# Kernel optimization log

Measured on AMD Instinct MI355X. Metric: run time of the kernel, lower is better.

The kernel has to match this reference:

```python
import jax, jax.numpy as jnp
import numpy as np

FEATURE_DIM = 128
EDGE_DIM = 32
N_NODES = 10000
BATCH = 4
N_EDGES = 640000
TEMPERATURE = 0.66
POWER_ITERS = 5


def spectral_normalize(W):
    # torch.nn.utils.spectral_norm: divide W by largest singular value estimated
    # via power iteration; u, v are treated as constants (no grad).
    # W: [out, in]
    u = jnp.ones((W.shape[0],), W.dtype) / jnp.sqrt(jnp.asarray(W.shape[0], W.dtype))
    for _ in range(POWER_ITERS):
        v = W.T @ u
        v = v / (jnp.linalg.norm(v) + 1e-12)
        u = W @ v
        u = u / (jnp.linalg.norm(u) + 1e-12)
    u = jax.lax.stop_gradient(u)
    v = jax.lax.stop_gradient(v)
    sigma = u @ (W @ v)
    return W / sigma


def setup_inputs() -> dict:
    key = jax.random.key(0)
    ks = jax.random.split(key, 8)
    node_feat = jax.random.normal(ks[0], (BATCH, N_NODES, FEATURE_DIM), dtype=jnp.float32)
    batch_ids = jax.random.randint(ks[1], (N_EDGES,), 0, BATCH)
    src_nodes = jax.random.randint(ks[2], (N_EDGES,), 0, N_NODES)
    tgt_nodes = jax.random.randint(ks[3], (N_EDGES,), 0, N_NODES)
    in_dim = 2 * FEATURE_DIM + 1  # src_feat ++ tgt_feat ++ distance
    # kaiming_normal_(nonlinearity='relu'): std = sqrt(2 / fan_in)
    W1 = jax.random.normal(ks[4], (EDGE_DIM, in_dim), jnp.float32) * np.sqrt(2.0 / in_dim)
    b1 = jnp.zeros((EDGE_DIM,), jnp.float32)
    W2 = jax.random.normal(ks[5], (EDGE_DIM, EDGE_DIM), jnp.float32) * np.sqrt(2.0 / EDGE_DIM)
    b2 = jnp.zeros((EDGE_DIM,), jnp.float32)
    bound = 0.1 * np.sqrt(6.0 / (EDGE_DIM + 1))
    W3 = jax.random.uniform(ks[6], (1, EDGE_DIM), jnp.float32, -bound, bound)
    b3 = jnp.ones((1,), jnp.float32)
    return {"node_feat": node_feat, "W1": W1, "b1": b1, "W2": W2, "b2": b2,
            "W3": W3, "b3": b3, "batch_ids": batch_ids,
            "src_nodes": src_nodes, "tgt_nodes": tgt_nodes}


def reference(node_feat, W1, b1, W2, b2, W3, b3, batch_ids, src_nodes, tgt_nodes):
    # per-edge gather of endpoint features  [E, D]
    src_feat = node_feat[batch_ids, src_nodes]
    tgt_feat = node_feat[batch_ids, tgt_nodes]
    dist = jnp.linalg.norm(src_feat - tgt_feat, axis=-1, keepdims=True)  # [E,1]
    edge_features = jnp.concatenate([src_feat, tgt_feat, dist], axis=-1)  # [E, 2D+1]
    # spectral-norm MLP (dropout is identity at eval / in this reference)
    h = jax.nn.relu(edge_features @ spectral_normalize(W1).T + b1)
    h = jax.nn.relu(h @ spectral_normalize(W2).T + b2)
    logAlpha = (h @ spectral_normalize(W3).T + b3).squeeze(-1)  # [E]
    logAlpha = jnp.clip(logAlpha, -5.0, 5.0)
    edge_weights = jax.nn.sigmoid(logAlpha / TEMPERATURE)
    return edge_weights, logAlpha
```

## Files before the change

### kernel.cpp

```cpp
#include <hip/hip_runtime.h>
#include <hip/hip_fp16.h>
#include <math.h>

#define FEATD 128
#define NNODES 10000
#define NBATCH 4
#define NROWS (NBATCH*NNODES)

#define OFF_I1   0
#define OFF_W1L  8
#define OFF_W2   64
#define OFF_W3   1088
#define OFF_W2H  1120
#define OFF_P16  4096
#define P16_FLOATS (NROWS*64/2)
#define OFF_FQ   (OFF_P16 + P16_FLOATS)
#define F16_FLOATS (NROWS*FEATD/2)
#define OFF_FBWT OFF_P16

#define WSTRIDE 68

typedef _Float16 h2 __attribute__((ext_vector_type(2)));
union U32H2 { unsigned u; h2 h; };
union U4H2  { uint4 u; h2 h[4]; };

#if defined(__has_builtin)
#if __has_builtin(__builtin_amdgcn_fdot2)
#define HAVE_FDOT2 1
#endif
#if __has_builtin(__builtin_amdgcn_cvt_pk_f32_fp8) && __has_builtin(__builtin_amdgcn_cvt_pk_fp8_f32)
#define HAVE_FP8 1
#endif
#endif

__device__ __forceinline__ float fdot2f(h2 a, h2 b, float c) {
#ifdef HAVE_FDOT2
  return __builtin_amdgcn_fdot2(a, b, c, false);
#else
  return c + (float)a[0] * (float)b[0] + (float)a[1] * (float)b[1];
#endif
}

#ifdef HAVE_FP8
typedef float floatx2 __attribute__((ext_vector_type(2)));
__device__ __forceinline__ float ssd_fp8_w(unsigned aw, unsigned bw, float s) {
  floatx2 al = __builtin_amdgcn_cvt_pk_f32_fp8((int)aw, false);
  floatx2 ah = __builtin_amdgcn_cvt_pk_f32_fp8((int)aw, true);
  floatx2 bl = __builtin_amdgcn_cvt_pk_f32_fp8((int)bw, false);
  floatx2 bh = __builtin_amdgcn_cvt_pk_f32_fp8((int)bw, true);
  float d0 = al[0] - bl[0], d1 = al[1] - bl[1];
  float d2 = ah[0] - bh[0], d3 = ah[1] - bh[1];
  return s + d0 * d0 + d1 * d1 + d2 * d2 + d3 * d3;
}
__device__ __forceinline__ float grp_dist_fp8(uint2 au, uint2 bu) {
  float ssd = ssd_fp8_w(au.x, bu.x, 0.f);
  ssd = ssd_fp8_w(au.y, bu.y, ssd);
  ssd += __shfl_xor(ssd, 1, 64);
  ssd += __shfl_xor(ssd, 2, 64);
  ssd += __shfl_xor(ssd, 4, 64);
  ssd += __shfl_xor(ssd, 8, 64);
  return sqrtf(ssd);
}
#endif

template <int M, int K>
__device__ float spectral_sigma_t(const float* __restrict__ Wg,
                                  float* sW, float* u, float* v, volatile float* red) {
  int tid = threadIdx.x;
  int wid = tid >> 6, lid = tid & 63;
  int j8 = tid >> 3, l8 = tid & 7;
  for (int i = tid; i < M * K; i += 256) sW[i] = Wg[i];
  if (tid < M) u[tid] = 1.0f;
  __syncthreads();
  float invu = 1.0f / sqrtf((float)M);
  float invv = 0.f;

  for (int it = 0; it < 5; ++it) {
    float p = 0.f;
    for (int k = tid; k < K; k += 256) {
      float a = 0.f;
      #pragma unroll
      for (int j = 0; j < M; ++j) a += sW[j * K + k] * u[j];
      a *= invu;
      v[k] = a;
      p += a * a;
    }
    #pragma unroll
    for (int off = 1; off < 64; off <<= 1) p += __shfl_xor(p, off, 64);
    if (lid == 0) red[wid] = p;
    __syncthreads();
    p = red[0] + red[1] + red[2] + red[3];
    invv = 1.0f / (sqrtf(p) + 1e-12f);

    float a = 0.f;
    if (j8 < M) {
      #pragma unroll
      for (int k = l8; k < K; k += 8) a += sW[j8 * K + k] * v[k];
      a *= invv;
    }
    a += __shfl_xor(a, 1, 64);
    a += __shfl_xor(a, 2, 64);
    a += __shfl_xor(a, 4, 64);
    float q = 0.f;
    if (j8 < M && l8 == 0) { u[j8] = a; q = a * a; }
    #pragma unroll
    for (int off = 1; off < 64; off <<= 1) q += __shfl_xor(q, off, 64);
    if (lid == 0) red[4 + wid] = q;
    __syncthreads();
    q = red[4] + red[5] + red[6] + red[7];
    invu = 1.0f / (sqrtf(q) + 1e-12f);
  }

  float a = 0.f;
  if (j8 < M) {
    #pragma unroll
    for (int k = l8; k < K; k += 8) a += sW[j8 * K + k] * v[k];
  }
  a += __shfl_xor(a, 1, 64);
  a += __shfl_xor(a, 2, 64);
  a += __shfl_xor(a, 4, 64);
  float s = (j8 < M && l8 == 0) ? a * u[j8] : 0.f;
  #pragma unroll
  for (int off = 1; off < 64; off <<= 1) s += __shfl_xor(s, off, 64);
  if (lid == 0) red[wid] = s;
  __syncthreads();
  float sig = (red[0] + red[1] + red[2] + red[3]) * invu * invv;
  __syncthreads();
  return sig;
}

__global__ __launch_bounds__(256, 4) void prep_kernel(const float* __restrict__ feat,
                                                      const float* __restrict__ W1,
                                                      const float* __restrict__ W2,
                                                      const float* __restrict__ W3,
                                                      float* __restrict__ ws,
                                                      int doFQ) {
  __shared__ float sA[128 * WSTRIDE];
  __shared__ float u[32], v[257];
  __shared__ float red[8];
  int tid = threadIdx.x;

  if (blockIdx.x == 0) {
    float sig1 = spectral_sigma_t<32, 257>(W1, sA, u, v, red);
    float i1 = 1.0f / sig1;
    if (tid == 0) ws[OFF_I1] = i1;
    for (int j = tid; j < 32; j += 256) ws[OFF_W1L + j] = sA[j * 257 + 256] * i1;
    __syncthreads();
    float sig2 = spectral_sigma_t<32, 32>(W2, sA, u, v, red);
    float i2 = 1.0f / sig2;
    for (int idx = tid; idx < 1024; idx += 256) ws[OFF_W2 + idx] = sA[idx] * i2;
    unsigned* w2h = (unsigned*)(ws + OFF_W2H);
    for (int idx = tid; idx < 512; idx += 256) {
      int j = idx >> 4, q = idx & 15;
      U32H2 pk;
      pk.h[0] = (_Float16)(sA[j * 32 + 2 * q] * i2);
      pk.h[1] = (_Float16)(sA[j * 32 + 2 * q + 1] * i2);
      w2h[idx] = pk.u;
    }
    __syncthreads();
    float sig3 = spectral_sigma_t<1, 32>(W3, sA, u, v, red);
    float i3 = 1.0f / sig3;
    for (int k = tid; k < 32; k += 256) ws[OFF_W3 + k] = sA[k] * i3;
    return;
  }

  for (int idx = tid; idx < 32 * 257; idx += 256) {
    int j = idx / 257, c = idx - j * 257;
    float w = W1[idx];
    if (c < 128) sA[c * WSTRIDE + j] = w;
    else if (c < 256) sA[(c - 128) * WSTRIDE + 32 + j] = w;
  }
  __syncthreads();

  __half* p16 = (__half*)(ws + OFF_P16);
  char* fq = (char*)(ws + OFF_FQ);
  int rg = tid >> 4;
  int jg = (tid & 15) << 2;
  int slice = tid & 15;
  int r0 = (blockIdx.x - 1) * 64 + rg * 4;
  const float4* F0 = (const float4*)&feat[(size_t)(r0 + 0) * FEATD];
  const float4* F1 = (const float4*)&feat[(size_t)(r0 + 1) * FEATD];
  const float4* F2 = (const float4*)&feat[(size_t)(r0 + 2) * FEATD];
  const float4* F3 = (const float4*)&feat[(size_t)(r0 + 3) * FEATD];
  float acc[4][4] = {{0,0,0,0},{0,0,0,0},{0,0,0,0},{0,0,0,0}};

  #pragma unroll 2
  for (int k4 = 0; k4 < 32; ++k4) {
    float4 f0 = F0[k4], f1 = F1[k4], f2 = F2[k4], f3 = F3[k4];
    if (doFQ && (k4 >> 1) == slice) {
#ifdef HAVE_FP8
      unsigned w;
      w = __builtin_amdgcn_cvt_pk_fp8_f32(f0.x, f0.y, 0, false);
      w = __builtin_amdgcn_cvt_pk_fp8_f32(f0.z, f0.w, (int)w, true);
      *(unsigned*)(fq + (size_t)(r0 + 0) * 128 + (size_t)k4 * 4) = w;
      w = __builtin_amdgcn_cvt_pk_fp8_f32(f1.x, f1.y, 0, false);
      w = __builtin_amdgcn_cvt_pk_fp8_f32(f1.z, f1.w, (int)w, true);
      *(unsigned*)(fq + (size_t)(r0 + 1) * 128 + (size_t)k4 * 4) = w;
      w = __builtin_amdgcn_cvt_pk_fp8_f32(f2.x, f2.y, 0, false);
      w = __builtin_amdgcn_cvt_pk_fp8_f32(f2.z, f2.w, (int)w, true);
      *(unsigned*)(fq + (size_t)(r0 + 2) * 128 + (size_t)k4 * 4) = w;
      w = __builtin_amdgcn_cvt_pk_fp8_f32(f3.x, f3.y, 0, false);
      w = __builtin_amdgcn_cvt_pk_fp8_f32(f3.z, f3.w, (int)w, true);
      *(unsigned*)(fq + (size_t)(r0 + 3) * 128 + (size_t)k4 * 4) = w;
#else
      U32H2 a, b; uint2 pk;
      a.h[0]=(_Float16)f0.x; a.h[1]=(_Float16)f0.y; b.h[0]=(_Float16)f0.z; b.h[1]=(_Float16)f0.w;
      pk.x=a.u; pk.y=b.u; *(uint2*)(fq + (size_t)(r0+0)*256 + (size_t)k4*8) = pk;
      a.h[0]=(_Float16)f1.x; a.h[1]=(_Float16)f1.y; b.h[0]=(_Float16)f1.z; b.h[1]=(_Float16)f1.w;
      pk.x=a.u; pk.y=b.u; *(uint2*)(fq + (size_t)(r0+1)*256 + (size_t)k4*8) = pk;
      a.h[0]=(_Float16)f2.x; a.h[1]=(_Float16)f2.y; b.h[0]=(_Float16)f2.z; b.h[1]=(_Float16)f2.w;
      pk.x=a.u; pk.y=b.u; *(uint2*)(fq + (size_t)(r0+2)*256 + (size_t)k4*8) = pk;
      a.h[0]=(_Float16)f3.x; a.h[1]=(_Float16)f3.y; b.h[0]=(_Float16)f3.z; b.h[1]=(_Float16)f3.w;
      pk.x=a.u; pk.y=b.u; *(uint2*)(fq + (size_t)(r0+3)*256 + (size_t)k4*8) = pk;
#endif
    }
    #pragma unroll
    for (int kk = 0; kk < 4; ++kk) {
      int k = 4 * k4 + kk;
      float4 w = *(const float4*)&sA[k * WSTRIDE + jg];
      float e0 = (kk == 0) ? f0.x : (kk == 1) ? f0.y : (kk == 2) ? f0.z : f0.w;
      float e1 = (kk == 0) ? f1.x : (kk == 1) ? f1.y : (kk == 2) ? f1.z : f1.w;
      float e2 = (kk == 0) ? f2.x : (kk == 1) ? f2.y : (kk == 2) ? f2.z : f2.w;
      float e3 = (kk == 0) ? f3.x : (kk == 1) ? f3.y : (kk == 2) ? f3.z : f3.w;
      acc[0][0] += e0 * w.x; acc[0][1] += e0 * w.y; acc[0][2] += e0 * w.z; acc[0][3] += e0 * w.w;
      acc[1][0] += e1 * w.x; acc[1][1] += e1 * w.y; acc[1][2] += e1 * w.z; acc[1][3] += e1 * w.w;
      acc[2][0] += e2 * w.x; acc[2][1] += e2 * w.y; acc[2][2] += e2 * w.z; acc[2][3] += e2 * w.w;
      acc[3][0] += e3 * w.x; acc[3][1] += e3 * w.y; acc[3][2] += e3 * w.z; acc[3][3] += e3 * w.w;
    }
  }
  #pragma unroll
  for (int r = 0; r < 4; ++r) {
    U32H2 a, b;
    a.h[0] = (_Float16)acc[r][0]; a.h[1] = (_Float16)acc[r][1];
    b.h[0] = (_Float16)acc[r][2]; b.h[1] = (_Float16)acc[r][3];
    uint2 o; o.x = a.u; o.y = b.u;
    *(uint2*)((char*)p16 + (size_t)(r0 + r) * 128 + (size_t)jg * 2) = o;
  }
}

__device__ __forceinline__ float grp_dist_f16(uint4 au, uint4 bu) {
  U4H2 a, b; a.u = au; b.u = bu;
  float ssd = 0.f;
  #pragma unroll
  for (int p = 0; p < 4; ++p) { h2 d = a.h[p] - b.h[p]; ssd = fdot2f(d, d, ssd); }
  ssd += __shfl_xor(ssd, 1, 64);
  ssd += __shfl_xor(ssd, 2, 64);
  ssd += __shfl_xor(ssd, 4, 64);
  ssd += __shfl_xor(ssd, 8, 64);
  return sqrtf(ssd);
}

__device__ __forceinline__ unsigned h1pack(unsigned puv, unsigned quv, float dist, float i1,
                                           float w1l0, float w1l1, float bb0, float bb1) {
  U32H2 p, q; p.u = puv; q.u = quv;
  float h0  = fmaxf(fmaf((float)p.h[0] + (float)q.h[0], i1, fmaf(dist, w1l0, bb0)), 0.f);
  float h1v = fmaxf(fmaf((float)p.h[1] + (float)q.h[1], i1, fmaf(dist, w1l1, bb1)), 0.f);
  U32H2 r; r.h[0] = (_Float16)h0; r.h[1] = (_Float16)h1v;
  return r.u;
}

template <bool FQ>
__global__ __launch_bounds__(256, 8) void edge_wave(const float* __restrict__ feat,
                                                    const float* __restrict__ ws,
                                                    const float* __restrict__ b1,
                                                    const float* __restrict__ b2,
                                                    const float* __restrict__ b3,
                                                    const int* __restrict__ bids,
                                                    const int* __restrict__ srcs,
                                                    const int* __restrict__ tgts,
                                                    float* __restrict__ out, int E) {
  __shared__ unsigned ht[4 * 64 * 17];
  int tid = threadIdx.x;
  int wv   = tid >> 6;
  int l64  = tid & 63;
  int grp  = l64 >> 4;
  int lane = l64 & 15;
  unsigned* htw = &ht[wv * 64 * 17];

  const char*  featq = (const char*)(ws + OFF_FQ);
  const __half* p16  = (const __half*)(ws + OFF_P16);
  const unsigned* w2h = (const unsigned*)(ws + OFF_W2H);

  float i1 = ws[OFF_I1];
  int j0 = 2 * lane;
  float w1l0 = ws[OFF_W1L + j0];
  float w1l1 = ws[OFF_W1L + j0 + 1];
  float bb0  = b1[j0];
  float bb1  = b1[j0 + 1];
  float bias3 = b3[0];

  int wstep = gridDim.x * 4 * 64;
  for (int base = (blockIdx.x * 4 + wv) * 64; base < E; base += wstep) {
    int e = base + l64;
    int rs_m = 0, rt_m = 0;
    if (e < E) {
      int b = bids[e];
      rs_m = b * NNODES + srcs[e];
      rt_m = b * NNODES + tgts[e];
    }

    if (FQ && (base + 64 <= E)) {
      int elb = grp << 4;
      #pragma unroll 1
      for (int rr = 0; rr < 4; ++rr) {
        int el0 = elb + 4 * rr + 0;
        int el1 = elb + 4 * rr + 1;
        int el2 = elb + 4 * rr + 2;
        int el3 = elb + 4 * rr + 3;
        int rs0 = __shfl(rs_m, el0, 64), rt0 = __shfl(rt_m, el0, 64);
        int rs1 = __shfl(rs_m, el1, 64), rt1 = __shfl(rt_m, el1, 64);
        int rs2 = __shfl(rs_m, el2, 64), rt2 = __shfl(rt_m, el2, 64);
        int rs3 = __shfl(rs_m, el3, 64), rt3 = __shfl(rt_m, el3, 64);
#ifdef HAVE_FP8
        uint2 a0 = *(const uint2*)(featq + ((size_t)rs0 << 7) + (lane << 3));
        uint2 c0 = *(const uint2*)(featq + ((size_t)rt0 << 7) + (lane << 3));
        uint2 a1 = *(const uint2*)(featq + ((size_t)rs1 << 7) + (lane << 3));
        uint2 c1 = *(const uint2*)(featq + ((size_t)rt1 << 7) + (lane << 3));
        uint2 a2 = *(const uint2*)(featq + ((size_t)rs2 << 7) + (lane << 3));
        uint2 c2 = *(const uint2*)(featq + ((size_t)rt2 << 7) + (lane << 3));
        uint2 a3 = *(const uint2*)(featq + ((size_t)rs3 << 7) + (lane << 3));
        uint2 c3 = *(const uint2*)(featq + ((size_t)rt3 << 7) + (lane << 3));
#else
        uint4 a0 = *(const uint4*)(featq + ((size_t)rs0 << 8) + (lane << 4));
        uint4 c0 = *(const uint4*)(featq + ((size_t)rt0 << 8) + (lane << 4));
        uint4 a1 = *(const uint4*)(featq + ((size_t)rs1 << 8) + (lane << 4));
        uint4 c1 = *(const uint4*)(featq + ((size_t)rt1 << 8) + (lane << 4));
        uint4 a2 = *(const uint4*)(featq + ((size_t)rs2 << 8) + (lane << 4));
        uint4 c2 = *(const uint4*)(featq + ((size_t)rt2 << 8) + (lane << 4));
        uint4 a3 = *(const uint4*)(featq + ((size_t)rs3 << 8) + (lane << 4));
        uint4 c3 = *(const uint4*)(featq + ((size_t)rt3 << 8) + (lane << 4));
#endif
        unsigned pu0 = *(const unsigned*)((const char*)p16 + ((size_t)rs0 << 7) + (lane << 2));
        unsigned qu0 = *(const unsigned*)((const char*)p16 + ((size_t)rt0 << 7) + 64 + (lane << 2));
        unsigned pu1 = *(const unsigned*)((const char*)p16 + ((size_t)rs1 << 7) + (lane << 2));
        unsigned qu1 = *(const unsigned*)((const char*)p16 + ((size_t)rt1 << 7) + 64 + (lane << 2));
        unsigned pu2 = *(const unsigned*)((const char*)p16 + ((size_t)rs2 << 7) + (lane << 2));
        unsigned qu2 = *(const unsigned*)((const char*)p16 + ((size_t)rt2 << 7) + 64 + (lane << 2));
        unsigned pu3 = *(const unsigned*)((const char*)p16 + ((size_t)rs3 << 7) + (lane << 2));
        unsigned qu3 = *(const unsigned*)((const char*)p16 + ((size_t)rt3 << 7) + 64 + (lane << 2));
#ifdef HAVE_FP8
        float d0 = grp_dist_fp8(a0, c0);
        float d1 = grp_dist_fp8(a1, c1);
        float d2 = grp_dist_fp8(a2, c2);
        float d3 = grp_dist_fp8(a3, c3);
#else
        float d0 = grp_dist_f16(a0, c0);
        float d1 = grp_dist_f16(a1, c1);
        float d2 = grp_dist_f16(a2, c2);
        float d3 = grp_dist_f16(a3, c3);
#endif
        htw[el0 * 17 + lane] = h1pack(pu0, qu0, d0, i1, w1l0, w1l1, bb0, bb1);
        htw[el1 * 17 + lane] = h1pack(pu1, qu1, d1, i1, w1l0, w1l1, bb0, bb1);
        htw[el2 * 17 + lane] = h1pack(pu2, qu2, d2, i1, w1l0, w1l1, bb0, bb1);
        htw[el3 * 17 + lane] = h1pack(pu3, qu3, d3, i1, w1l0, w1l1, bb0, bb1);
      }
    } else {
      int elb = grp << 4;
      #pragma unroll 2
      for (int r = 0; r < 16; ++r) {
        int el = elb + r;
        if (base + el < E) {
          int rs = __shfl(rs_m, el, 64), rt = __shfl(rt_m, el, 64);
          float dist;
          if (FQ) {
#ifdef HAVE_FP8
            uint2 au = *(const uint2*)(featq + ((size_t)rs << 7) + (lane << 3));
            uint2 bu = *(const uint2*)(featq + ((size_t)rt << 7) + (lane << 3));
            dist = grp_dist_fp8(au, bu);
#else
            uint4 au = *(const uint4*)(featq + ((size_t)rs << 8) + (lane << 4));
            uint4 bu = *(const uint4*)(featq + ((size_t)rt << 8) + (lane << 4));
            dist = grp_dist_f16(au, bu);
#endif
          } else {
            const float4* A  = (const float4*)&feat[(size_t)rs * FEATD];
            const float4* Bp = (const float4*)&feat[(size_t)rt * FEATD];
            float ssd = 0.f;
            #pragma unroll
            for (int p = 0; p < 2; ++p) {
              float4 a = A[lane * 2 + p], c = Bp[lane * 2 + p];
              float dx = a.x - c.x, dy = a.y - c.y, dz = a.z - c.z, dw = a.w - c.w;
              ssd += dx * dx + dy * dy + dz * dz + dw * dw;
            }
            ssd += __shfl_xor(ssd, 1, 64);
            ssd += __shfl_xor(ssd, 2, 64);
            ssd += __shfl_xor(ssd, 4, 64);
            ssd += __shfl_xor(ssd, 8, 64);
            dist = sqrtf(ssd);
          }
          unsigned puv = *(const unsigned*)((const char*)p16 + ((size_t)rs << 7) + (lane << 2));
          unsigned quv = *(const unsigned*)((const char*)p16 + ((size_t)rt << 7) + 64 + (lane << 2));
          htw[el * 17 + lane] = h1pack(puv, quv, dist, i1, w1l0, w1l1, bb0, bb1);
        }
      }
    }

    if (e < E) {
      unsigned hrow[16];
      #pragma unroll
      for (int q = 0; q < 16; ++q) hrow[q] = htw[l64 * 17 + q];
      float la = bias3;
      #pragma unroll
      for (int j = 0; j < 32; ++j) {
        float acc = b2[j];
        #pragma unroll
        for (int q = 0; q < 16; ++q) {
          U32H2 w; w.u = w2h[j * 16 + q];
          U32H2 h; h.u = hrow[q];
          acc = fdot2f(w.h, h.h, acc);
        }
        la += ws[OFF_W3 + j] * fmaxf(acc, 0.f);
      }
      la = fminf(fmaxf(la, -5.f), 5.f);
      out[e]     = 1.0f / (1.0f + exp2f(la * -2.18590179f));
      out[E + e] = la;
    }
  }
}

__global__ __launch_bounds__(256) void spectral_full(const float* __restrict__ W1,
                                                     const float* __restrict__ W2,
                                                     const float* __restrict__ W3,
                                                     float* __restrict__ ws) {
  __shared__ float sA[32 * 257];
  __shared__ float u[32], v[257];
  __shared__ float red[8];
  int tid = threadIdx.x;
  float sig1 = spectral_sigma_t<32, 257>(W1, sA, u, v, red);
  float i1 = 1.0f / sig1;
  for (int idx = tid; idx < 128 * 64; idx += 256) {
    int k = idx >> 6, jj = idx & 63;
    float w = (jj < 32) ? sA[jj * 257 + k] : sA[(jj - 32) * 257 + 128 + k];
    ws[OFF_FBWT + idx] = w * i1;
  }
  for (int j = tid; j < 32; j += 256) ws[OFF_W1L + j] = sA[j * 257 + 256] * i1;
  __syncthreads();
  float sig2 = spectral_sigma_t<32, 32>(W2, sA, u, v, red);
  float i2 = 1.0f / sig2;
  for (int idx = tid; idx < 1024; idx += 256) ws[OFF_W2 + idx] = sA[idx] * i2;
  __syncthreads();
  float sig3 = spectral_sigma_t<1, 32>(W3, sA, u, v, red);
  float i3 = 1.0f / sig3;
  for (int k = tid; k < 32; k += 256) ws[OFF_W3 + k] = sA[k] * i3;
}

__global__ __launch_bounds__(256) void edge_kernel_nop(const float* __restrict__ feat,
                                                       const float* __restrict__ ws,
                                                       const float* __restrict__ b1,
                                                       const float* __restrict__ b2,
                                                       const float* __restrict__ b3,
                                                       const int* __restrict__ bids,
                                                       const int* __restrict__ srcs,
                                                       const int* __restrict__ tgts,
                                                       float* __restrict__ out, int E) {
  __shared__ float sWt[128 * 64];
  __shared__ float sW2[1024];
  __shared__ float sW3[32], sW1l[32], sB1[32], sB2[32];
  int tid = threadIdx.x;
  for (int i = tid * 4; i < 128 * 64; i += 256 * 4)
    *(float4*)&sWt[i] = *(const float4*)&ws[OFF_FBWT + i];
  for (int i = tid; i < 1024; i += 256) sW2[i] = ws[OFF_W2 + i];
  if (tid < 32) {
    sW3[tid]  = ws[OFF_W3 + tid];
    sW1l[tid] = ws[OFF_W1L + tid];
    sB1[tid]  = b1[tid];
    sB2[tid]  = b2[tid];
  }
  __syncthreads();
  float bias3 = b3[0];

  for (int e = blockIdx.x * 256 + tid; e < E; e += gridDim.x * 256) {
    int b = bids[e], s = srcs[e], t = tgts[e];
    const float4* A  = (const float4*)&feat[(size_t)(b * NNODES + s) * FEATD];
    const float4* Bp = (const float4*)&feat[(size_t)(b * NNODES + t) * FEATD];
    float ssd = 0.f;
    float h1p[32];
    #pragma unroll
    for (int j = 0; j < 32; ++j) h1p[j] = 0.f;
    #pragma unroll 1
    for (int k4 = 0; k4 < 32; ++k4) {
      float4 a = A[k4], c = Bp[k4];
      float dx = a.x - c.x, dy = a.y - c.y, dz = a.z - c.z, dw = a.w - c.w;
      ssd += dx * dx + dy * dy + dz * dz + dw * dw;
      #pragma unroll
      for (int kk = 0; kk < 4; ++kk) {
        int k = 4 * k4 + kk;
        float fa = (kk == 0) ? a.x : (kk == 1) ? a.y : (kk == 2) ? a.z : a.w;
        float fc = (kk == 0) ? c.x : (kk == 1) ? c.y : (kk == 2) ? c.z : c.w;
        #pragma unroll
        for (int q = 0; q < 8; ++q) {
          float4 w0 = *(const float4*)&sWt[k * 64 + 4 * q];
          float4 w1 = *(const float4*)&sWt[k * 64 + 32 + 4 * q];
          h1p[4*q+0] += fa * w0.x + fc * w1.x;
          h1p[4*q+1] += fa * w0.y + fc * w1.y;
          h1p[4*q+2] += fa * w0.z + fc * w1.z;
          h1p[4*q+3] += fa * w0.w + fc * w1.w;
        }
      }
    }
    float dist = sqrtf(ssd);
    float h1[32];
    #pragma unroll
    for (int j = 0; j < 32; ++j)
      h1[j] = fmaxf(h1p[j] + dist * sW1l[j] + sB1[j], 0.f);
    float la = bias3;
    #pragma unroll
    for (int j = 0; j < 32; ++j) {
      float acc = sB2[j];
      #pragma unroll
      for (int q = 0; q < 8; ++q) {
        float4 w = *(const float4*)&sW2[j * 32 + 4 * q];
        acc += w.x * h1[4 * q] + w.y * h1[4 * q + 1] + w.z * h1[4 * q + 2] + w.w * h1[4 * q + 3];
      }
      la += sW3[j] * fmaxf(acc, 0.f);
    }
    la = fminf(fmaxf(la, -5.f), 5.f);
    out[e]     = 1.0f / (1.0f + __expf(-la / 0.66f));
    out[E + e] = la;
  }
}

extern "C" void kernel_launch(void* const* d_in, const int* in_sizes, int n_in,
                              void* d_out, int out_size, void* d_ws, size_t ws_size,
                              hipStream_t stream) {
  const float* feat = (const float*)d_in[0];
  const float* W1   = (const float*)d_in[1];
  const float* b1   = (const float*)d_in[2];
  const float* W2   = (const float*)d_in[3];
  const float* b2   = (const float*)d_in[4];
  const float* W3   = (const float*)d_in[5];
  const float* b3   = (const float*)d_in[6];
  const int* bids   = (const int*)d_in[7];
  const int* srcs   = (const int*)d_in[8];
  const int* tgts   = (const int*)d_in[9];
  float* out = (float*)d_out;
  float* ws  = (float*)d_ws;
  int E = in_sizes[7];

  size_t need_p  = (size_t)OFF_FQ * sizeof(float);
  size_t need_fq = (size_t)(OFF_FQ + F16_FLOATS) * sizeof(float);
  int egrid = (E + 255) / 256;

  if (ws_size >= need_fq) {
    prep_kernel<<<dim3(626), dim3(256), 0, stream>>>(feat, W1, W2, W3, ws, 1);
    edge_wave<true><<<dim3(egrid), dim3(256), 0, stream>>>(feat, ws, b1, b2, b3,
                                                           bids, srcs, tgts, out, E);
  } else if (ws_size >= need_p) {
    prep_kernel<<<dim3(626), dim3(256), 0, stream>>>(feat, W1, W2, W3, ws, 0);
    edge_wave<false><<<dim3(egrid), dim3(256), 0, stream>>>(feat, ws, b1, b2, b3,
                                                            bids, srcs, tgts, out, E);
  } else {
    spectral_full<<<dim3(1), dim3(256), 0, stream>>>(W1, W2, W3, ws);
    edge_kernel_nop<<<dim3(egrid), dim3(256), 0, stream>>>(feat, ws, b1, b2, b3,
                                                           bids, srcs, tgts, out, E);
  }
}
```

Measured before the change: 91.56 us.

## Compute second MLP layer with MFMA 16x16x32 f16 instead of fdot2 loops

Replaces the per-lane scalar fdot2 evaluation of the 32x32 second layer with two MFMA 16x16x32 f16 ops per 16-edge tile. W2 fragments are preloaded into registers, and the layer-3 dot product is reduced with xor shuffles across 16 lanes. The shared-memory row stride is padded to 20 words so 16-byte fragment loads stay aligned. The aim is to cut VALU work in the edge MLP, at the cost of extra shuffles and a fallback path for partial tiles.

```diff
diff --git a/kernel.cpp b/kernel.cpp
--- a/kernel.cpp
+++ b/kernel.cpp
@@ -19,10 +19,14 @@
 #define OFF_FBWT OFF_P16
 
 #define WSTRIDE 68
+#define ASTRIDE 20
 
 typedef _Float16 h2 __attribute__((ext_vector_type(2)));
+typedef _Float16 h8v __attribute__((ext_vector_type(8)));
+typedef float f4v __attribute__((ext_vector_type(4)));
 union U32H2 { unsigned u; h2 h; };
 union U4H2  { uint4 u; h2 h[4]; };
+union U4H8  { uint4 u; h8v h; };
 
 #if defined(__has_builtin)
 #if __has_builtin(__builtin_amdgcn_fdot2)
@@ -30,6 +34,9 @@
 #endif
 #if __has_builtin(__builtin_amdgcn_cvt_pk_f32_fp8) && __has_builtin(__builtin_amdgcn_cvt_pk_fp8_f32)
 #define HAVE_FP8 1
+#endif
+#if __has_builtin(__builtin_amdgcn_mfma_f32_16x16x32_f16)
+#define HAVE_MFMA16 1
 #endif
 #endif
 
@@ -269,13 +276,13 @@
                                                     const int* __restrict__ srcs,
                                                     const int* __restrict__ tgts,
                                                     float* __restrict__ out, int E) {
-  __shared__ unsigned ht[4 * 64 * 17];
+  __shared__ unsigned sAh[4 * 64 * ASTRIDE];
   int tid = threadIdx.x;
   int wv   = tid >> 6;
   int l64  = tid & 63;
   int grp  = l64 >> 4;
   int lane = l64 & 15;
-  unsigned* htw = &ht[wv * 64 * 17];
+  unsigned* htw = &sAh[wv * 64 * ASTRIDE];
 
   const char*  featq = (const char*)(ws + OFF_FQ);
   const __half* p16  = (const __half*)(ws + OFF_P16);
@@ -288,6 +295,16 @@
   float bb0  = b1[j0];
   float bb1  = b1[j0 + 1];
   float bias3 = b3[0];
+
+#ifdef HAVE_MFMA16
+  int q4 = l64 >> 4;
+  int nc = l64 & 15;
+  float b2n0 = b2[nc], b2n1 = b2[16 + nc];
+  float w3n0 = ws[OFF_W3 + nc], w3n1 = ws[OFF_W3 + 16 + nc];
+  U4H8 Bf0, Bf1;
+  Bf0.u = *(const uint4*)&w2h[nc * 16 + q4 * 4];
+  Bf1.u = *(const uint4*)&w2h[(16 + nc) * 16 + q4 * 4];
+#endif
 
   int wstep = gridDim.x * 4 * 64;
   for (int base = (blockIdx.x * 4 + wv) * 64; base < E; base += wstep) {
@@ -298,8 +315,9 @@
       rs_m = b * NNODES + srcs[e];
       rt_m = b * NNODES + tgts[e];
     }
-
-    if (FQ && (base + 64 <= E)) {
+    bool full = (base + 64 <= E);
+
+    if (FQ && full) {
       int elb = grp << 4;
       #pragma unroll 1
       for (int rr = 0; rr < 4; ++rr) {
@@ -349,10 +367,10 @@
         float d2 = grp_dist_f16(a2, c2);
         float d3 = grp_dist_f16(a3, c3);
 #endif
-        htw[el0 * 17 + lane] = h1pack(pu0, qu0, d0, i1, w1l0, w1l1, bb0, bb1);
-        htw[el1 * 17 + lane] = h1pack(pu1, qu1, d1, i1, w1l0, w1l1, bb0, bb1);
-        htw[el2 * 17 + lane] = h1pack(pu2, qu2, d2, i1, w1l0, w1l1, bb0, bb1);
-        htw[el3 * 17 + lane] = h1pack(pu3, qu3, d3, i1, w1l0, w1l1, bb0, bb1);
+        htw[el0 * ASTRIDE + lane] = h1pack(pu0, qu0, d0, i1, w1l0, w1l1, bb0, bb1);
+        htw[el1 * ASTRIDE + lane] = h1pack(pu1, qu1, d1, i1, w1l0, w1l1, bb0, bb1);
+        htw[el2 * ASTRIDE + lane] = h1pack(pu2, qu2, d2, i1, w1l0, w1l1, bb0, bb1);
+        htw[el3 * ASTRIDE + lane] = h1pack(pu3, qu3, d3, i1, w1l0, w1l1, bb0, bb1);
       }
     } else {
       int elb = grp << 4;
@@ -390,30 +408,67 @@
           }
           unsigned puv = *(const unsigned*)((const char*)p16 + ((size_t)rs << 7) + (lane << 2));
           unsigned quv = *(const unsigned*)((const char*)p16 + ((size_t)rt << 7) + 64 + (lane << 2));
-          htw[el * 17 + lane] = h1pack(puv, quv, dist, i1, w1l0, w1l1, bb0, bb1);
+          htw[el * ASTRIDE + lane] = h1pack(puv, quv, dist, i1, w1l0, w1l1, bb0, bb1);
         }
       }
     }
 
-    if (e < E) {
-      unsigned hrow[16];
+#ifdef HAVE_MFMA16
+    if (full) {
       #pragma unroll
-      for (int q = 0; q < 16; ++q) hrow[q] = htw[l64 * 17 + q];
-      float la = bias3;
-      #pragma unroll
-      for (int j = 0; j < 32; ++j) {
-        float acc = b2[j];
+      for (int mt = 0; mt < 4; ++mt) {
+        int medge = mt * 16 + nc;
+        U4H8 Af;
+        Af.u = *(const uint4*)&htw[medge * ASTRIDE + q4 * 4];
+        f4v acc0 = {b2n0, b2n0, b2n0, b2n0};
+        f4v acc1 = {b2n1, b2n1, b2n1, b2n1};
+        acc0 = __builtin_amdgcn_mfma_f32_16x16x32_f16(Af.h, Bf0.h, acc0, 0, 0, 0);
+        acc1 = __builtin_amdgcn_mfma_f32_16x16x32_f16(Af.h, Bf1.h, acc1, 0, 0, 0);
+        float p0 = w3n0 * fmaxf(acc0[0], 0.f) + w3n1 * fmaxf(acc1[0], 0.f);
+        float p1 = w3n0 * fmaxf(acc0[1], 0.f) + w3n1 * fmaxf(acc1[1], 0.f);
+        float p2 = w3n0 * fmaxf(acc0[2], 0.f) + w3n1 * fmaxf(acc1[2], 0.f);
+        float p3 = w3n0 * fmaxf(acc0[3], 0.f) + w3n1 * fmaxf(acc1[3], 0.f);
         #pragma unroll
-        for (int q = 0; q < 16; ++q) {
-          U32H2 w; w.u = w2h[j * 16 + q];
-          U32H2 h; h.u = hrow[q];
-          acc = fdot2f(w.h, h.h, acc);
+        for (int off = 1; off < 16; off <<= 1) {
+          p0 += __shfl_xor(p0, off, 64);
+          p1 += __shfl_xor(p1, off, 64);
+          p2 += __shfl_xor(p2, off, 64);
+          p3 += __shfl_xor(p3, off, 64);
         }
-        la += ws[OFF_W3 + j] * fmaxf(acc, 0.f);
+        int c = nc;
+        if (c < 8) {
+          int i = c & 3;
+          float la = (i == 0) ? p0 : (i == 1) ? p1 : (i == 2) ? p2 : p3;
+          la += bias3;
+          la = fminf(fmaxf(la, -5.f), 5.f);
+          int eo = base + mt * 16 + (q4 << 2) + i;
+          if (c < 4) out[eo] = 1.0f / (1.0f + exp2f(la * -2.18590179f));
+          else       out[E + eo] = la;
+        }
       }
-      la = fminf(fmaxf(la, -5.f), 5.f);
-      out[e]     = 1.0f / (1.0f + exp2f(la * -2.18590179f));
-      out[E + e] = la;
+    } else
+#endif
+    {
+      if (e < E) {
+        unsigned hrow[16];
+        #pragma unroll
+        for (int q = 0; q < 16; ++q) hrow[q] = htw[l64 * ASTRIDE + q];
+        float la = bias3;
+        #pragma unroll
+        for (int j = 0; j < 32; ++j) {
+          float acc = b2[j];
+          #pragma unroll
+          for (int q = 0; q < 16; ++q) {
+            U32H2 w; w.u = w2h[j * 16 + q];
+            U32H2 h; h.u = hrow[q];
+            acc = fdot2f(w.h, h.h, acc);
+          }
+          la += ws[OFF_W3 + j] * fmaxf(acc, 0.f);
+        }
+        la = fminf(fmaxf(la, -5.f), 5.f);
+        out[e]     = 1.0f / (1.0f + exp2f(la * -2.18590179f));
+        out[E + e] = la;
+      }
     }
   }
 }
```

Result: slower. 102.3 us (+11.8%).
